# Kernel tuning notes

Measured on AMD Instinct MI355X. Metric: run time of the kernel, lower is better.

Reference implementation:

```python
import jax, jax.numpy as jnp
import numpy as np

B, T, N, D, L, TE, F, H = 32, 1024, 256, 512, 512, 512, 2048, 8

PARAM_SHAPES = {
    "sa_norm_g": (D,), "sa_norm_b": (D,),
    "sa_q_w": (D, D), "sa_q_b": (D,), "sa_k_w": (D, D), "sa_k_b": (D,), "sa_v_w": (D, D), "sa_v_b": (D,),
    "sa_emb_w": (TE, 2 * D), "sa_emb_b": (2 * D,), "sa_pnorm_g": (D,), "sa_pnorm_b": (D,),
    "sa_out_w": (D, D), "sa_out_b": (D,),
    "ca_norm_g": (D,), "ca_norm_b": (D,), "ca_tnorm_g": (L,), "ca_tnorm_b": (L,),
    "ca_q_w": (D, D), "ca_q_b": (D,), "ca_k_w": (L, D), "ca_k_b": (D,), "ca_v_w": (L, D), "ca_v_b": (D,),
    "ca_emb_w": (TE, 2 * D), "ca_emb_b": (2 * D,), "ca_pnorm_g": (D,), "ca_pnorm_b": (D,),
    "ca_out_w": (D, D), "ca_out_b": (D,),
    "ffn_w1": (D, F), "ffn_b1": (F,), "ffn_w2": (F, D), "ffn_b2": (D,),
    "ffn_emb_w": (TE, 2 * D), "ffn_emb_b": (2 * D,), "ffn_pnorm_g": (D,), "ffn_pnorm_b": (D,),
    "ffn_out_w": (D, D), "ffn_out_b": (D,),
}


def setup_inputs() -> dict:
    key = jax.random.key(0)
    inp = {}
    inp["x"] = jax.random.normal(jax.random.fold_in(key, 100), (B, T, D), jnp.float32)
    inp["xf"] = jax.random.normal(jax.random.fold_in(key, 101), (B, N, L), jnp.float32)
    inp["emb"] = jax.random.normal(jax.random.fold_in(key, 102), (B, TE), jnp.float32)
    inp["src_mask"] = (jax.random.uniform(jax.random.fold_in(key, 103), (B, T, 1)) < 0.9).astype(jnp.float32)
    for i, (name, shp) in enumerate(PARAM_SHAPES.items()):
        k = jax.random.fold_in(key, i)
        if name.endswith("norm_g") or name.endswith("pnorm_g") or name.endswith("tnorm_g"):
            inp[name] = jnp.ones(shp, jnp.float32)
        else:
            inp[name] = 0.02 * jax.random.normal(k, shp, jnp.float32)
    return inp


def _ln(v, g, b):
    mu = jnp.mean(v, -1, keepdims=True)
    var = jnp.mean(jnp.square(v - mu), -1, keepdims=True)
    return (v - mu) * jax.lax.rsqrt(var + 1e-5) * g + b


def _styl(h, emb, ew, eb, ng, nb, ow, ob):
    # StylizationBlock: AdaLN scale-shift then SiLU + linear (dropout = identity at eval)
    e = (jax.nn.silu(emb) @ ew + eb)[:, None, :]          # [B, 1, 2D]
    scale, shift = jnp.split(e, 2, axis=-1)
    hn = _ln(h, ng, nb) * (1.0 + scale) + shift
    return jax.nn.silu(hn) @ ow + ob


def _lin_attn(q, k, v):
    # Performer-style: contract over sequence first -> [B,H,d,dl], then apply queries
    att = jnp.einsum('bnhd,bnhl->bhdl', k, v)
    return jnp.einsum('bthd,bhdl->bthl', q, att)


def _forward(x, xf, emb, src_mask, sa_norm_g, sa_norm_b, sa_q_w, sa_q_b, sa_k_w, sa_k_b, sa_v_w, sa_v_b, sa_emb_w, sa_emb_b, sa_pnorm_g, sa_pnorm_b, sa_out_w, sa_out_b, ca_norm_g, ca_norm_b, ca_tnorm_g, ca_tnorm_b, ca_q_w, ca_q_b, ca_k_w, ca_k_b, ca_v_w, ca_v_b, ca_emb_w, ca_emb_b, ca_pnorm_g, ca_pnorm_b, ca_out_w, ca_out_b, ffn_w1, ffn_b1, ffn_w2, ffn_b2, ffn_emb_w, ffn_emb_b, ffn_pnorm_g, ffn_pnorm_b, ffn_out_w, ffn_out_b):
    B_, T_, D_ = x.shape
    d = D_ // H
    # ---- linear temporal self-attention ----
    xn = _ln(x, sa_norm_g, sa_norm_b)
    q = jax.nn.softmax((xn @ sa_q_w + sa_q_b).reshape(B_, T_, H, d), axis=-1)   # softmax over feature dim
    k = jax.nn.softmax((xn @ sa_k_w + sa_k_b + (1.0 - src_mask) * -1000000.0).reshape(B_, T_, H, d), axis=1)  # softmax over seq
    v = ((xn @ sa_v_w + sa_v_b) * src_mask).reshape(B_, T_, H, d)
    y = _lin_attn(q, k, v).reshape(B_, T_, D_)
    x = x + _styl(y, emb, sa_emb_w, sa_emb_b, sa_pnorm_g, sa_pnorm_b, sa_out_w, sa_out_b)
    # ---- linear temporal cross-attention ----
    xn = _ln(x, ca_norm_g, ca_norm_b)
    tn = _ln(xf, ca_tnorm_g, ca_tnorm_b)
    N_ = xf.shape[1]
    q = jax.nn.softmax((xn @ ca_q_w + ca_q_b).reshape(B_, T_, H, d), axis=-1)
    k = jax.nn.softmax((tn @ ca_k_w + ca_k_b).reshape(B_, N_, H, d), axis=1)
    v = (tn @ ca_v_w + ca_v_b).reshape(B_, N_, H, d)
    y = _lin_attn(q, k, v).reshape(B_, T_, D_)
    x = x + _styl(y, emb, ca_emb_w, ca_emb_b, ca_pnorm_g, ca_pnorm_b, ca_out_w, ca_out_b)
    # ---- FFN ----
    y = jax.nn.gelu(x @ ffn_w1 + ffn_b1, approximate=False) @ ffn_w2 + ffn_b2
    x = x + _styl(y, emb, ffn_emb_w, ffn_emb_b, ffn_pnorm_g, ffn_pnorm_b, ffn_out_w, ffn_out_b)
    return x


def reference(x, xf, emb, src_mask, sa_norm_g, sa_norm_b, sa_q_w, sa_q_b, sa_k_w, sa_k_b, sa_v_w, sa_v_b, sa_emb_w, sa_emb_b, sa_pnorm_g, sa_pnorm_b, sa_out_w, sa_out_b, ca_norm_g, ca_norm_b, ca_tnorm_g, ca_tnorm_b, ca_q_w, ca_q_b, ca_k_w, ca_k_b, ca_v_w, ca_v_b, ca_emb_w, ca_emb_b, ca_pnorm_g, ca_pnorm_b, ca_out_w, ca_out_b, ffn_w1, ffn_b1, ffn_w2, ffn_b2, ffn_emb_w, ffn_emb_b, ffn_pnorm_g, ffn_pnorm_b, ffn_out_w, ffn_out_b):
    return _forward(x, xf, emb, src_mask, sa_norm_g, sa_norm_b, sa_q_w, sa_q_b, sa_k_w, sa_k_b, sa_v_w, sa_v_b, sa_emb_w, sa_emb_b, sa_pnorm_g, sa_pnorm_b, sa_out_w, sa_out_b, ca_norm_g, ca_norm_b, ca_tnorm_g, ca_tnorm_b, ca_q_w, ca_q_b, ca_k_w, ca_k_b, ca_v_w, ca_v_b, ca_emb_w, ca_emb_b, ca_pnorm_g, ca_pnorm_b, ca_out_w, ca_out_b, ffn_w1, ffn_b1, ffn_w2, ffn_b2, ffn_emb_w, ffn_emb_b, ffn_pnorm_g, ffn_pnorm_b, ffn_out_w, ffn_out_b)
```

## Files before the change

### kernel.cpp

```cpp
#include <hip/hip_runtime.h>
#include <hip/hip_bf16.h>
#include <math.h>

typedef __hip_bfloat16 bf16;
typedef __hip_bfloat162 bf16x2;
using s8 = __attribute__((ext_vector_type(8))) short;
using h4 = __attribute__((ext_vector_type(4))) short;
using f4 = __attribute__((ext_vector_type(4))) float;

#define DEV __device__ __forceinline__
DEV float bf2f(bf16 h){ return __bfloat162float(h); }
DEV bf16  f2bf(float f){ return __float2bfloat16(f); }
DEV float silu_f(float x){ return x / (1.0f + __expf(-x)); }
DEV float gelu_f(float x){
  float z = 1.5957691216f * x * (1.0f + 0.044715f * x * x);
  return x / (1.0f + __expf(-z));
}

struct TDesc { const float* src; bf16* dst; int K; int N; int tiles; };
struct TPack { TDesc d[11]; };
__global__ __launch_bounds__(256) void transpose_all(TPack p){
  int tile = blockIdx.x;
  int i = 0, base = 0;
  while (i < 10 && tile >= base + p.d[i].tiles){ base += p.d[i].tiles; ++i; }
  int local = tile - base;
  const float* in = p.d[i].src;
  bf16* out = p.d[i].dst;
  int K = p.d[i].K, N = p.d[i].N;
  int ntx = N >> 5;
  int n0 = (local % ntx) * 32, k0 = (local / ntx) * 32;
  __shared__ float t[32][33];
  int tx = threadIdx.x, ty = threadIdx.y;
  for (int r = ty; r < 32; r += 8) t[r][tx] = in[(size_t)(k0 + r) * N + n0 + tx];
  __syncthreads();
  for (int r = ty; r < 32; r += 8) out[(size_t)(n0 + r) * K + k0 + tx] = f2bf(t[tx][r]);
}

__global__ __launch_bounds__(256) void concat_bias(const float* __restrict__ qb, const float* __restrict__ kb,
                                                   const float* __restrict__ vb, const float* __restrict__ ckb,
                                                   const float* __restrict__ cvb,
                                                   float* __restrict__ sab, float* __restrict__ cab){
  int t = blockIdx.x * 256 + threadIdx.x;
  if (t < 512){ sab[t] = qb[t]; cab[t] = ckb[t]; cab[512 + t] = cvb[t]; }
  else if (t < 1024){ sab[t] = kb[t - 512]; }
  else if (t < 1536){ sab[t] = vb[t - 1024]; }
}

__global__ __launch_bounds__(256) void ln_kernel(const float* __restrict__ in, bf16* __restrict__ out,
                                                 const float* __restrict__ g, const float* __restrict__ b){
  int row = blockIdx.x * 4 + (threadIdx.x >> 6);
  int lane = threadIdx.x & 63;
  const float* r = in + (size_t)row * 512 + lane * 8;
  float4 v0 = *(const float4*)r;
  float4 v1 = *(const float4*)(r + 4);
  float f[8] = {v0.x, v0.y, v0.z, v0.w, v1.x, v1.y, v1.z, v1.w};
  float s = 0.0f, s2 = 0.0f;
  #pragma unroll
  for (int j = 0; j < 8; ++j){ s += f[j]; s2 += f[j] * f[j]; }
  #pragma unroll
  for (int o = 1; o < 64; o <<= 1){ s += __shfl_xor(s, o); s2 += __shfl_xor(s2, o); }
  float mu = s * (1.0f / 512.0f);
  float var = fmaxf(s2 * (1.0f / 512.0f) - mu * mu, 0.0f);
  float rstd = rsqrtf(var + 1e-5f);
  int c = lane * 8;
  s8 o;
  #pragma unroll
  for (int j = 0; j < 8; ++j)
    ((bf16*)&o)[j] = f2bf((f[j] - mu) * rstd * g[c + j] + b[c + j]);
  *(s8*)&out[(size_t)row * 512 + c] = o;
}

__global__ __launch_bounds__(256) void styl_ln_kernel(const bf16* __restrict__ in, const float* __restrict__ e,
                                                      const float* __restrict__ g, const float* __restrict__ b,
                                                      bf16* __restrict__ out, int T){
  int row = blockIdx.x * 4 + (threadIdx.x >> 6);
  int lane = threadIdx.x & 63;
  int bidx = row / T;
  int c = lane * 8;
  s8 hv = *(const s8*)&in[(size_t)row * 512 + c];
  float f[8];
  float s = 0.0f, s2 = 0.0f;
  #pragma unroll
  for (int j = 0; j < 8; ++j){
    f[j] = bf2f(((const bf16*)&hv)[j]);
    s += f[j]; s2 += f[j] * f[j];
  }
  #pragma unroll
  for (int o = 1; o < 64; o <<= 1){ s += __shfl_xor(s, o); s2 += __shfl_xor(s2, o); }
  float mu = s * (1.0f / 512.0f);
  float var = fmaxf(s2 * (1.0f / 512.0f) - mu * mu, 0.0f);
  float rstd = rsqrtf(var + 1e-5f);
  const float* eb = e + (size_t)bidx * 1024;
  s8 o;
  #pragma unroll
  for (int j = 0; j < 8; ++j){
    float h = (f[j] - mu) * rstd * g[c + j] + b[c + j];
    h = h * (1.0f + eb[c + j]) + eb[512 + c + j];
    ((bf16*)&o)[j] = f2bf(silu_f(h));
  }
  *(s8*)&out[(size_t)row * 512 + c] = o;
}

__global__ __launch_bounds__(256) void kv_outer(const bf16* __restrict__ k, const bf16* __restrict__ v,
                                                const float* __restrict__ mask,
                                                float* __restrict__ att_part, float* __restrict__ den_part,
                                                int T, int ld, int Tc){
  int bh = blockIdx.x;
  int b = bh >> 3, h = bh & 7;
  int chunk = blockIdx.y;
  int t_begin = chunk * Tc;
  __shared__ float kexp[64][64];
  __shared__ bf16 vb[64][64];
  int tid = threadIdx.x;
  int lg = tid & 15, tg = tid >> 4;
  int d0 = tg * 4, l0 = lg * 4;
  const float* mrow = mask ? (mask + (size_t)b * T) : nullptr;
  float acc[4][4] = {};
  float sden[4] = {0.0f, 0.0f, 0.0f, 0.0f};
  for (int tcb = t_begin; tcb < t_begin + Tc; tcb += 64){
    __syncthreads();
    #pragma unroll
    for (int i = 0; i < 2; ++i){
      int rr = (tid >> 3) + i * 32;
      int cc = (tid & 7) * 8;
      size_t goff = ((size_t)(b * T + tcb + rr)) * ld + h * 64 + cc;
      s8 kv8 = *(const s8*)&k[goff];
      *(s8*)&vb[rr][cc] = *(const s8*)&v[goff];
      float mk = mrow ? mrow[tcb + rr] : 1.0f;
      float4 e0, e1;
      e0.x = mk * __expf(bf2f(((const bf16*)&kv8)[0]));
      e0.y = mk * __expf(bf2f(((const bf16*)&kv8)[1]));
      e0.z = mk * __expf(bf2f(((const bf16*)&kv8)[2]));
      e0.w = mk * __expf(bf2f(((const bf16*)&kv8)[3]));
      e1.x = mk * __expf(bf2f(((const bf16*)&kv8)[4]));
      e1.y = mk * __expf(bf2f(((const bf16*)&kv8)[5]));
      e1.z = mk * __expf(bf2f(((const bf16*)&kv8)[6]));
      e1.w = mk * __expf(bf2f(((const bf16*)&kv8)[7]));
      *(float4*)&kexp[rr][cc]     = e0;
      *(float4*)&kexp[rr][cc + 4] = e1;
    }
    __syncthreads();
    for (int tt = 0; tt < 64; ++tt){
      float4 kf = *(const float4*)&kexp[tt][d0];
      float kk[4] = {kf.x, kf.y, kf.z, kf.w};
      h4 vv4 = *(const h4*)&vb[tt][l0];
      float vv[4];
      #pragma unroll
      for (int j = 0; j < 4; ++j) vv[j] = bf2f(((const bf16*)&vv4)[j]);
      #pragma unroll
      for (int a = 0; a < 4; ++a){
        sden[a] += kk[a];
        #pragma unroll
        for (int c2 = 0; c2 < 4; ++c2) acc[a][c2] += kk[a] * vv[c2];
      }
    }
  }
  size_t base = ((size_t)(chunk * 256 + bh)) * 4096;
  #pragma unroll
  for (int a = 0; a < 4; ++a)
    #pragma unroll
    for (int c2 = 0; c2 < 4; ++c2) att_part[base + (size_t)(d0 + a) * 64 + l0 + c2] = acc[a][c2];
  if (lg == 0){
    size_t dbase = ((size_t)(chunk * 256 + bh)) * 64;
    #pragma unroll
    for (int a = 0; a < 4; ++a) den_part[dbase + d0 + a] = sden[a];
  }
}

__global__ __launch_bounds__(256) void kv_reduce(const float* __restrict__ att_part,
                                                 const float* __restrict__ den_part,
                                                 float* __restrict__ att, int nchunk){
  int bh = blockIdx.x, tid = threadIdx.x;
  __shared__ float dinv[64];
  if (tid < 64){
    float d = 0.0f;
    for (int c = 0; c < nchunk; ++c) d += den_part[((size_t)(c * 256 + bh)) * 64 + tid];
    dinv[tid] = 1.0f / d;
  }
  __syncthreads();
  #pragma unroll
  for (int i = 0; i < 16; ++i){
    int e = i * 256 + tid;
    float s = 0.0f;
    for (int c = 0; c < nchunk; ++c) s += att_part[((size_t)(c * 256 + bh)) * 4096 + e];
    att[(size_t)bh * 4096 + e] = s * dinv[e >> 6];
  }
}

__global__ __launch_bounds__(256) void q_att(const bf16* __restrict__ q, const float* __restrict__ att,
                                             bf16* __restrict__ y, int T, int ldq){
  int ntc = T >> 6;
  int idx = blockIdx.x;
  int tcb = idx % ntc; int h = (idx / ntc) & 7; int b = idx / (ntc * 8);
  __shared__ float ab[64][64];
  __shared__ bf16 qb[64][64];
  int tid = threadIdx.x;
  #pragma unroll
  for (int i = 0; i < 4; ++i){
    int e = i * 1024 + tid * 4;
    *(float4*)&ab[e >> 6][e & 63] = *(const float4*)&att[((size_t)(b * 8 + h)) * 4096 + e];
  }
  #pragma unroll
  for (int i = 0; i < 2; ++i){
    int rr = (tid >> 3) + i * 32;
    int cc = (tid & 7) * 8;
    s8 v = *(const s8*)&q[((size_t)(b * T + tcb * 64 + rr)) * ldq + h * 64 + cc];
    float f[8];
    #pragma unroll
    for (int j = 0; j < 8; ++j) f[j] = bf2f(((const bf16*)&v)[j]);
    float m = f[0];
    #pragma unroll
    for (int j = 1; j < 8; ++j) m = fmaxf(m, f[j]);
    m = fmaxf(m, __shfl_xor(m, 1));
    m = fmaxf(m, __shfl_xor(m, 2));
    m = fmaxf(m, __shfl_xor(m, 4));
    float s = 0.0f;
    #pragma unroll
    for (int j = 0; j < 8; ++j){ f[j] = __expf(f[j] - m); s += f[j]; }
    s += __shfl_xor(s, 1);
    s += __shfl_xor(s, 2);
    s += __shfl_xor(s, 4);
    float inv = 1.0f / s;
    s8 o;
    #pragma unroll
    for (int j = 0; j < 8; ++j) ((bf16*)&o)[j] = f2bf(f[j] * inv);
    *(s8*)&qb[rr][cc ^ ((rr & 7) << 3)] = o;
  }
  __syncthreads();
  int lg = tid & 15, tg = tid >> 4;
  int t0 = tg * 4, l0 = lg * 4;
  float acc[4][4] = {};
  for (int d8 = 0; d8 < 64; d8 += 8){
    s8 qrow[4];
    #pragma unroll
    for (int j = 0; j < 4; ++j){
      int row = t0 + j;
      qrow[j] = *(const s8*)&qb[row][d8 ^ ((row & 7) << 3)];
    }
    #pragma unroll
    for (int e = 0; e < 8; ++e){
      float4 av4 = *(const float4*)&ab[d8 + e][l0];
      float av[4] = {av4.x, av4.y, av4.z, av4.w};
      #pragma unroll
      for (int a = 0; a < 4; ++a){
        float qv = bf2f(((const bf16*)&qrow[a])[e]);
        #pragma unroll
        for (int c2 = 0; c2 < 4; ++c2) acc[a][c2] += qv * av[c2];
      }
    }
  }
  #pragma unroll
  for (int a = 0; a < 4; ++a)
    #pragma unroll
    for (int c2 = 0; c2 < 4; ++c2)
      y[((size_t)(b * T + tcb * 64 + t0 + a)) * 512 + h * 64 + l0 + c2] = f2bf(acc[a][c2]);
}

__global__ __launch_bounds__(256) void emb_gemm(const float* __restrict__ emb,
    const float* __restrict__ w0, const float* __restrict__ b0,
    const float* __restrict__ w1, const float* __restrict__ b1,
    const float* __restrict__ w2, const float* __restrict__ b2,
    float* __restrict__ e_all){
  int col = blockIdx.x * 256 + threadIdx.x;
  int b = blockIdx.y, which = blockIdx.z;
  const float* W  = (which == 0) ? w0 : (which == 1 ? w1 : w2);
  const float* bb = (which == 0) ? b0 : (which == 1 ? b1 : b2);
  __shared__ float s[512];
  for (int i = threadIdx.x; i < 512; i += 256){ float v = emb[b * 512 + i]; s[i] = silu_f(v); }
  __syncthreads();
  float acc = bb[col];
  for (int kk = 0; kk < 512; ++kk) acc += s[kk] * W[(size_t)kk * 1024 + col];
  e_all[((size_t)which * 32 + b) * 1024 + col] = acc;
}

template<int EPI>
__global__ __launch_bounds__(256, 2) void gemm_bt(
    const bf16* __restrict__ A, const bf16* __restrict__ BT,
    const float* __restrict__ bias, void* __restrict__ out,
    const float* __restrict__ extra, void* __restrict__ out2, int M, int N, int K){
  constexpr bool SW = (EPI == 3 || EPI == 4 || EPI == 5);
  __shared__ __align__(16) bf16 As[2][128 * 32];
  __shared__ __align__(16) bf16 Bs[2][128 * 32];
  int tid = threadIdx.x;
  int w = tid >> 6, lane = tid & 63;
  int wr = w >> 1, wc = w & 1;
  int nwg = gridDim.x * gridDim.y;
  int lin = blockIdx.y * gridDim.x + blockIdx.x;
  int xcd = lin & 7, sidx = lin >> 3;
  int q8 = nwg >> 3, r8 = nwg & 7;
  int wg = (xcd < r8 ? xcd * (q8 + 1) : r8 * (q8 + 1) + (xcd - r8) * q8) + sidx;
  int bn = wg % gridDim.x, bm = wg / gridDim.x;

  const bf16* Ab = A  + (size_t)bm * 128 * K;
  const bf16* Bb = BT + (size_t)bn * 128 * K;

  int srow = tid >> 2;
  int scol = (tid & 3) * 8;

  auto stage = [&](int buf, int k0){
    #pragma unroll
    for (int i = 0; i < 2; ++i){
      const bf16* ga = Ab + (size_t)(srow + i * 64) * K + k0 + scol;
      const bf16* gb = Bb + (size_t)(srow + i * 64) * K + k0 + scol;
      bf16* la = &As[buf][i * 2048 + w * 512];
      bf16* lb = &Bs[buf][i * 2048 + w * 512];
      __builtin_amdgcn_global_load_lds((const __attribute__((address_space(1))) void*)ga,
                                       (__attribute__((address_space(3))) void*)la, 16, 0, 0);
      __builtin_amdgcn_global_load_lds((const __attribute__((address_space(1))) void*)gb,
                                       (__attribute__((address_space(3))) void*)lb, 16, 0, 0);
    }
  };

  f4 acc[4][4];
  #pragma unroll
  for (int m = 0; m < 4; ++m)
    #pragma unroll
    for (int n = 0; n < 4; ++n)
      #pragma unroll
      for (int j = 0; j < 4; ++j) acc[m][n][j] = 0.0f;

  int nt = K >> 5;
  int arow = lane & 15;
  int koff = (lane >> 4) * 8;

  stage(0, 0);
  __syncthreads();
  int cur = 0;
  for (int t = 0; t < nt; ++t){
    if (t + 1 < nt) stage(cur ^ 1, (t + 1) * 32);
    s8 af[4], bfv[4];
    #pragma unroll
    for (int m = 0; m < 4; ++m)
      af[m] = *(const s8*)&As[cur][(wr * 64 + m * 16 + arow) * 32 + koff];
    #pragma unroll
    for (int n = 0; n < 4; ++n)
      bfv[n] = *(const s8*)&Bs[cur][(wc * 64 + n * 16 + arow) * 32 + koff];
    #pragma unroll
    for (int m = 0; m < 4; ++m)
      #pragma unroll
      for (int n = 0; n < 4; ++n){
        if constexpr (SW)
          acc[m][n] = __builtin_amdgcn_mfma_f32_16x16x32_bf16(bfv[n], af[m], acc[m][n], 0, 0, 0);
        else
          acc[m][n] = __builtin_amdgcn_mfma_f32_16x16x32_bf16(af[m], bfv[n], acc[m][n], 0, 0, 0);
      }
    __syncthreads();
    cur ^= 1;
  }

  if constexpr (SW){
    int rbase = bm * 128 + wr * 64 + (lane & 15);
    int cbase = bn * 128 + wc * 64 + (lane >> 4) * 4;
    #pragma unroll
    for (int m = 0; m < 4; ++m){
      int row = rbase + m * 16;
      #pragma unroll
      for (int n = 0; n < 4; ++n){
        int col = cbase + n * 16;
        float4 bv = *(const float4*)&bias[col];
        float v0 = acc[m][n][0] + bv.x;
        float v1 = acc[m][n][1] + bv.y;
        float v2 = acc[m][n][2] + bv.z;
        float v3 = acc[m][n][3] + bv.w;
        size_t oi = (size_t)row * N + col;
        if (EPI == 3){
          float4* po = (float4*)&((float*)out)[oi];
          float4 c = *po;
          c.x += v0; c.y += v1; c.z += v2; c.w += v3;
          *po = c;
        } else if (EPI == 4){
          float4 e = *(const float4*)&extra[oi];
          float4 r = {e.x + v0, e.y + v1, e.z + v2, e.w + v3};
          *(float4*)&((float*)out)[oi] = r;
        } else {
          float4* po = (float4*)&((float*)out)[oi];
          float4 c = *po;
          c.x += v0; c.y += v1; c.z += v2; c.w += v3;
          *po = c;
          h4 o;
          ((bf16*)&o)[0] = f2bf(c.x); ((bf16*)&o)[1] = f2bf(c.y);
          ((bf16*)&o)[2] = f2bf(c.z); ((bf16*)&o)[3] = f2bf(c.w);
          *(h4*)&((bf16*)out2)[oi] = o;
        }
      }
    }
  } else {
    int r0 = bm * 128 + wr * 64 + (lane >> 4) * 4;
    int c0 = bn * 128 + wc * 64 + (lane & 15);
    #pragma unroll
    for (int m = 0; m < 4; ++m){
      #pragma unroll
      for (int n = 0; n < 4; ++n){
        int col = c0 + n * 16;
        float bv = bias[col];
        #pragma unroll
        for (int j = 0; j < 4; ++j){
          int row = r0 + m * 16 + j;
          float v = acc[m][n][j] + bv;
          size_t oi = (size_t)row * N + col;
          if (EPI == 0){
            ((bf16*)out)[oi] = f2bf(v);
          } else if (EPI == 2){
            ((bf16*)out)[oi] = f2bf(gelu_f(v));
          } else {
            float sc = (col >= 1024) ? extra[row] : 1.0f;
            ((bf16*)out)[oi] = f2bf(v * sc);
          }
        }
      }
    }
  }
}

extern "C" void kernel_launch(void* const* d_in, const int* in_sizes, int n_in,
                              void* d_out, int out_size, void* d_ws, size_t ws_size,
                              hipStream_t stream){
  const float* x    = (const float*)d_in[0];
  const float* xf   = (const float*)d_in[1];
  const float* emb  = (const float*)d_in[2];
  const float* mask = (const float*)d_in[3];
  const float* P[40];
  for (int j = 0; j < 40; ++j) P[j] = (const float*)d_in[4 + j];
  enum { SA_NG, SA_NB, SA_QW, SA_QB, SA_KW, SA_KB, SA_VW, SA_VB, SA_EW, SA_EB, SA_PG, SA_PB, SA_OW, SA_OB,
         CA_NG, CA_NB, CA_TG, CA_TB, CA_QW, CA_QB, CA_KW, CA_KB, CA_VW, CA_VB, CA_EW, CA_EB, CA_PG, CA_PB, CA_OW, CA_OB,
         F_W1, F_B1, F_W2, F_B2, F_EW, F_EB, F_PG, F_PB, F_OW, F_OB };

  char* wp = (char*)d_ws;
  auto alloc = [&](size_t bytes){ void* p = (void*)wp; wp += (bytes + 255) & ~(size_t)255; return p; };

  const size_t SQ = (size_t)512 * 512 * 2;
  bf16* WT_saqkv = (bf16*)alloc(3 * SQ);
  bf16* WT_saout = (bf16*)alloc(SQ);
  bf16* WT_caq   = (bf16*)alloc(SQ);
  bf16* WT_cakv  = (bf16*)alloc(2 * SQ);
  bf16* WT_caout = (bf16*)alloc(SQ);
  bf16* WT_f1    = (bf16*)alloc((size_t)2048 * 512 * 2);
  bf16* WT_f2    = (bf16*)alloc((size_t)512 * 2048 * 2);
  bf16* WT_fout  = (bf16*)alloc(SQ);
  float* cat_sab = (float*)alloc(1536 * 4);
  float* cat_cab = (float*)alloc(1024 * 4);
  float* e_all   = (float*)alloc((size_t)3 * 32 * 1024 * 4);

  const size_t BTD2 = (size_t)32768 * 512 * 2;
  bf16* bxn  = (bf16*)alloc(BTD2);
  bf16* bqkv = (bf16*)alloc(3 * BTD2);
  bf16* by   = (bf16*)alloc(BTD2);
  bf16* bs   = (bf16*)alloc(BTD2);
  bf16* btn  = (bf16*)alloc((size_t)8192 * 512 * 2);
  float* att_part = (float*)alloc((size_t)4 * 256 * 4096 * 4);
  float* den_part = (float*)alloc((size_t)4 * 256 * 64 * 4);
  float* batt = (float*)alloc((size_t)256 * 4096 * 4);
  bf16* bh1 = bxn;
  bf16* bq_ca  = bqkv;
  bf16* bkv_ca = bqkv + BTD2 / 2;

  TPack tp;
  auto set = [&](int i, const float* s, bf16* d, int K, int N){
    tp.d[i].src = s; tp.d[i].dst = d; tp.d[i].K = K; tp.d[i].N = N;
    tp.d[i].tiles = (K >> 5) * (N >> 5);
  };
  set(0,  P[SA_QW], WT_saqkv,              512, 512);
  set(1,  P[SA_KW], WT_saqkv + 512 * 512,  512, 512);
  set(2,  P[SA_VW], WT_saqkv + 1024 * 512, 512, 512);
  set(3,  P[SA_OW], WT_saout,              512, 512);
  set(4,  P[CA_QW], WT_caq,                512, 512);
  set(5,  P[CA_KW], WT_cakv,               512, 512);
  set(6,  P[CA_VW], WT_cakv + 512 * 512,   512, 512);
  set(7,  P[CA_OW], WT_caout,              512, 512);
  set(8,  P[F_OW],  WT_fout,               512, 512);
  set(9,  P[F_W1],  WT_f1,                 512, 2048);
  set(10, P[F_W2],  WT_f2,                 2048, 512);
  int total_tiles = 9 * 256 + 1024 + 1024;
  transpose_all<<<total_tiles, dim3(32, 8), 0, stream>>>(tp);

  concat_bias<<<6, 256, 0, stream>>>(P[SA_QB], P[SA_KB], P[SA_VB], P[CA_KB], P[CA_VB], cat_sab, cat_cab);

  emb_gemm<<<dim3(4, 32, 3), 256, 0, stream>>>(emb, P[SA_EW], P[SA_EB], P[CA_EW], P[CA_EB],
                                               P[F_EW], P[F_EB], e_all);

  dim3 g512(4, 256);

  ln_kernel<<<8192, 256, 0, stream>>>(x, bxn, P[SA_NG], P[SA_NB]);
  gemm_bt<6><<<dim3(12, 256), 256, 0, stream>>>(bxn, WT_saqkv, cat_sab, bqkv, mask, nullptr, 32768, 1536, 512);
  kv_outer<<<dim3(256, 4), 256, 0, stream>>>(bqkv + 512, bqkv + 1024, mask, att_part, den_part, 1024, 1536, 256);
  kv_reduce<<<256, 256, 0, stream>>>(att_part, den_part, batt, 4);
  q_att<<<4096, 256, 0, stream>>>(bqkv, batt, by, 1024, 1536);
  styl_ln_kernel<<<8192, 256, 0, stream>>>(by, e_all, P[SA_PG], P[SA_PB], bs, 1024);
  gemm_bt<4><<<g512, 256, 0, stream>>>(bs, WT_saout, P[SA_OB], d_out, x, nullptr, 32768, 512, 512);

  ln_kernel<<<8192, 256, 0, stream>>>((const float*)d_out, bxn, P[CA_NG], P[CA_NB]);
  ln_kernel<<<2048, 256, 0, stream>>>(xf, btn, P[CA_TG], P[CA_TB]);
  gemm_bt<0><<<g512, 256, 0, stream>>>(bxn, WT_caq, P[CA_QB], bq_ca, nullptr, nullptr, 32768, 512, 512);
  gemm_bt<0><<<dim3(8, 64), 256, 0, stream>>>(btn, WT_cakv, cat_cab, bkv_ca, nullptr, nullptr, 8192, 1024, 512);
  kv_outer<<<dim3(256, 2), 256, 0, stream>>>(bkv_ca, bkv_ca + 512, nullptr, att_part, den_part, 256, 1024, 128);
  kv_reduce<<<256, 256, 0, stream>>>(att_part, den_part, batt, 2);
  q_att<<<4096, 256, 0, stream>>>(bq_ca, batt, by, 1024, 512);
  styl_ln_kernel<<<8192, 256, 0, stream>>>(by, e_all + 32 * 1024, P[CA_PG], P[CA_PB], bs, 1024);
  gemm_bt<5><<<g512, 256, 0, stream>>>(bs, WT_caout, P[CA_OB], d_out, nullptr, by, 32768, 512, 512);

  gemm_bt<2><<<dim3(16, 256), 256, 0, stream>>>(by, WT_f1, P[F_B1], bh1, nullptr, nullptr, 32768, 2048, 512);
  gemm_bt<0><<<dim3(4, 256), 256, 0, stream>>>(bh1, WT_f2, P[F_B2], bs, nullptr, nullptr, 32768, 512, 2048);
  styl_ln_kernel<<<8192, 256, 0, stream>>>(bs, e_all + 2 * 32 * 1024, P[F_PG], P[F_PB], by, 1024);
  gemm_bt<3><<<g512, 256, 0, stream>>>(by, WT_fout, P[F_OB], d_out, nullptr, nullptr, 32768, 512, 512);
}
```

Before: 778.8 us.

## Keep residual stream in bf16 between sublayers instead of fp32 d_out

```diff
diff --git a/kernel.cpp b/kernel.cpp
--- a/kernel.cpp
+++ b/kernel.cpp
@@ -63,6 +63,31 @@
   float var = fmaxf(s2 * (1.0f / 512.0f) - mu * mu, 0.0f);
   float rstd = rsqrtf(var + 1e-5f);
   int c = lane * 8;
+  s8 o;
+  #pragma unroll
+  for (int j = 0; j < 8; ++j)
+    ((bf16*)&o)[j] = f2bf((f[j] - mu) * rstd * g[c + j] + b[c + j]);
+  *(s8*)&out[(size_t)row * 512 + c] = o;
+}
+
+__global__ __launch_bounds__(256) void ln_bf16_kernel(const bf16* __restrict__ in, bf16* __restrict__ out,
+                                                      const float* __restrict__ g, const float* __restrict__ b){
+  int row = blockIdx.x * 4 + (threadIdx.x >> 6);
+  int lane = threadIdx.x & 63;
+  int c = lane * 8;
+  s8 hv = *(const s8*)&in[(size_t)row * 512 + c];
+  float f[8];
+  float s = 0.0f, s2 = 0.0f;
+  #pragma unroll
+  for (int j = 0; j < 8; ++j){
+    f[j] = bf2f(((const bf16*)&hv)[j]);
+    s += f[j]; s2 += f[j] * f[j];
+  }
+  #pragma unroll
+  for (int o = 1; o < 64; o <<= 1){ s += __shfl_xor(s, o); s2 += __shfl_xor(s2, o); }
+  float mu = s * (1.0f / 512.0f);
+  float var = fmaxf(s2 * (1.0f / 512.0f) - mu * mu, 0.0f);
+  float rstd = rsqrtf(var + 1e-5f);
   s8 o;
   #pragma unroll
   for (int j = 0; j < 8; ++j)
@@ -278,7 +303,7 @@
     const bf16* __restrict__ A, const bf16* __restrict__ BT,
     const float* __restrict__ bias, void* __restrict__ out,
     const float* __restrict__ extra, void* __restrict__ out2, int M, int N, int K){
-  constexpr bool SW = (EPI == 3 || EPI == 4 || EPI == 5);
+  constexpr bool SW = (EPI == 9);
   __shared__ __align__(16) bf16 As[2][128 * 32];
   __shared__ __align__(16) bf16 Bs[2][128 * 32];
   int tid = threadIdx.x;
@@ -358,30 +383,14 @@
       for (int n = 0; n < 4; ++n){
         int col = cbase + n * 16;
         float4 bv = *(const float4*)&bias[col];
-        float v0 = acc[m][n][0] + bv.x;
-        float v1 = acc[m][n][1] + bv.y;
-        float v2 = acc[m][n][2] + bv.z;
-        float v3 = acc[m][n][3] + bv.w;
         size_t oi = (size_t)row * N + col;
-        if (EPI == 3){
-          float4* po = (float4*)&((float*)out)[oi];
-          float4 c = *po;
-          c.x += v0; c.y += v1; c.z += v2; c.w += v3;
-          *po = c;
-        } else if (EPI == 4){
-          float4 e = *(const float4*)&extra[oi];
-          float4 r = {e.x + v0, e.y + v1, e.z + v2, e.w + v3};
-          *(float4*)&((float*)out)[oi] = r;
-        } else {
-          float4* po = (float4*)&((float*)out)[oi];
-          float4 c = *po;
-          c.x += v0; c.y += v1; c.z += v2; c.w += v3;
-          *po = c;
-          h4 o;
-          ((bf16*)&o)[0] = f2bf(c.x); ((bf16*)&o)[1] = f2bf(c.y);
-          ((bf16*)&o)[2] = f2bf(c.z); ((bf16*)&o)[3] = f2bf(c.w);
-          *(h4*)&((bf16*)out2)[oi] = o;
-        }
+        h4 e4 = *(const h4*)&((const bf16*)extra)[oi];
+        float4 r;
+        r.x = bf2f(((const bf16*)&e4)[0]) + acc[m][n][0] + bv.x;
+        r.y = bf2f(((const bf16*)&e4)[1]) + acc[m][n][1] + bv.y;
+        r.z = bf2f(((const bf16*)&e4)[2]) + acc[m][n][2] + bv.z;
+        r.w = bf2f(((const bf16*)&e4)[3]) + acc[m][n][3] + bv.w;
+        *(float4*)&((float*)out)[oi] = r;
       }
     }
   } else {
@@ -402,6 +411,10 @@
             ((bf16*)out)[oi] = f2bf(v);
           } else if (EPI == 2){
             ((bf16*)out)[oi] = f2bf(gelu_f(v));
+          } else if (EPI == 7){
+            ((bf16*)out)[oi] = f2bf(extra[oi] + v);
+          } else if (EPI == 8){
+            ((bf16*)out)[oi] = f2bf(bf2f(((const bf16*)extra)[oi]) + v);
           } else {
             float sc = (col >= 1024) ? extra[row] : 1.0f;
             ((bf16*)out)[oi] = f2bf(v * sc);
@@ -450,7 +463,7 @@
   float* att_part = (float*)alloc((size_t)4 * 256 * 4096 * 4);
   float* den_part = (float*)alloc((size_t)4 * 256 * 64 * 4);
   float* batt = (float*)alloc((size_t)256 * 4096 * 4);
-  bf16* bh1 = bxn;
+  bf16* bh1 = bqkv;
   bf16* bq_ca  = bqkv;
   bf16* bkv_ca = bqkv + BTD2 / 2;
 
@@ -486,20 +499,20 @@
   kv_reduce<<<256, 256, 0, stream>>>(att_part, den_part, batt, 4);
   q_att<<<4096, 256, 0, stream>>>(bqkv, batt, by, 1024, 1536);
   styl_ln_kernel<<<8192, 256, 0, stream>>>(by, e_all, P[SA_PG], P[SA_PB], bs, 1024);
-  gemm_bt<4><<<g512, 256, 0, stream>>>(bs, WT_saout, P[SA_OB], d_out, x, nullptr, 32768, 512, 512);
-
-  ln_kernel<<<8192, 256, 0, stream>>>((const float*)d_out, bxn, P[CA_NG], P[CA_NB]);
+  gemm_bt<7><<<g512, 256, 0, stream>>>(bs, WT_saout, P[SA_OB], bxn, x, nullptr, 32768, 512, 512);
+
+  ln_bf16_kernel<<<8192, 256, 0, stream>>>(bxn, by, P[CA_NG], P[CA_NB]);
   ln_kernel<<<2048, 256, 0, stream>>>(xf, btn, P[CA_TG], P[CA_TB]);
-  gemm_bt<0><<<g512, 256, 0, stream>>>(bxn, WT_caq, P[CA_QB], bq_ca, nullptr, nullptr, 32768, 512, 512);
+  gemm_bt<0><<<g512, 256, 0, stream>>>(by, WT_caq, P[CA_QB], bq_ca, nullptr, nullptr, 32768, 512, 512);
   gemm_bt<0><<<dim3(8, 64), 256, 0, stream>>>(btn, WT_cakv, cat_cab, bkv_ca, nullptr, nullptr, 8192, 1024, 512);
   kv_outer<<<dim3(256, 2), 256, 0, stream>>>(bkv_ca, bkv_ca + 512, nullptr, att_part, den_part, 256, 1024, 128);
   kv_reduce<<<256, 256, 0, stream>>>(att_part, den_part, batt, 2);
   q_att<<<4096, 256, 0, stream>>>(bq_ca, batt, by, 1024, 512);
   styl_ln_kernel<<<8192, 256, 0, stream>>>(by, e_all + 32 * 1024, P[CA_PG], P[CA_PB], bs, 1024);
-  gemm_bt<5><<<g512, 256, 0, stream>>>(bs, WT_caout, P[CA_OB], d_out, nullptr, by, 32768, 512, 512);
-
-  gemm_bt<2><<<dim3(16, 256), 256, 0, stream>>>(by, WT_f1, P[F_B1], bh1, nullptr, nullptr, 32768, 2048, 512);
+  gemm_bt<8><<<g512, 256, 0, stream>>>(bs, WT_caout, P[CA_OB], bxn, (const float*)bxn, nullptr, 32768, 512, 512);
+
+  gemm_bt<2><<<dim3(16, 256), 256, 0, stream>>>(bxn, WT_f1, P[F_B1], bh1, nullptr, nullptr, 32768, 2048, 512);
   gemm_bt<0><<<dim3(4, 256), 256, 0, stream>>>(bh1, WT_f2, P[F_B2], bs, nullptr, nullptr, 32768, 512, 2048);
   styl_ln_kernel<<<8192, 256, 0, stream>>>(bs, e_all + 2 * 32 * 1024, P[F_PG], P[F_PB], by, 1024);
-  gemm_bt<3><<<g512, 256, 0, stream>>>(by, WT_fout, P[F_OB], d_out, nullptr, nullptr, 32768, 512, 512);
-}
+  gemm_bt<9><<<g512, 256, 0, stream>>>(by, WT_fout, P[F_OB], d_out, (const float*)bxn, nullptr, 32768, 512, 512);
+}
```

Measured after the change: 731.3 us. 1.07x faster.
